# Performance work log

Measured on AMD Instinct MI355X. Metric: run time of the kernel, lower is better.

The kernel has to match this reference:

```python
import jax, jax.numpy as jnp
import numpy as np

B, S, E = 8, 8192, 1024  # batch, seq_len, embed_dim (= n_wires)


def _rx(psi, th):
    # psi: (E, 2) complex64, th: scalar/(1,)/(E,)
    c = jnp.cos(0.5 * th)
    s = jnp.sin(0.5 * th)
    a, b = psi[..., 0], psi[..., 1]
    return jnp.stack([c * a - 1j * s * b, -1j * s * a + c * b], axis=-1)


def _ry(psi, th):
    c = jnp.cos(0.5 * th)
    s = jnp.sin(0.5 * th)
    a, b = psi[..., 0], psi[..., 1]
    return jnp.stack([c * a - s * b, s * a + c * b], axis=-1)


def _rz(psi, th):
    p = jnp.exp(-0.5j * th.astype(jnp.complex64))
    a, b = psi[..., 0], psi[..., 1]
    return jnp.stack([p * a, jnp.conj(p) * b], axis=-1)


def setup_inputs() -> dict:
    key = jax.random.key(0)
    ks = jax.random.split(key, 9)
    return {
        "x": jax.random.normal(ks[0], (B, S, E), dtype=jnp.float32),
        "bs_theta": jax.random.normal(ks[1], (1,), dtype=jnp.float32) * 0.5,
        "bs_phi": jax.random.normal(ks[2], (1,), dtype=jnp.float32) * 0.5,
        "phases": jax.random.normal(ks[3], (E,), dtype=jnp.float32),
        "squeeze_r": jax.random.normal(ks[4], (E,), dtype=jnp.float32),
        "displacement_r": jax.random.normal(ks[5], (E,), dtype=jnp.float32),
        "kerr": jax.random.normal(ks[6], (E,), dtype=jnp.float32),
        "W_combine": jax.random.normal(ks[7], (E, E), dtype=jnp.float32) / np.sqrt(E),
        "b_combine": jax.random.normal(ks[8], (E,), dtype=jnp.float32) * 0.01,
    }


def reference(x, bs_theta, bs_phi, phases, squeeze_r, displacement_r, kerr,
              W_combine, b_combine):
    e = x.shape[-1]
    # One qubit per embedding wire, all starting at |0>; gates are single-wire,
    # so the 2^E product state factorizes exactly into (E, 2) amplitudes.
    psi = jnp.zeros((e, 2), dtype=jnp.complex64).at[:, 0].set(1.0)
    psi = _rx(psi, bs_theta)          # rx(bs_theta) on every wire
    psi = _ry(psi, bs_phi)            # ry(bs_phi)
    psi = _rz(psi, phases)            # rz(phases[i])
    psi = _ry(psi, squeeze_r)         # ry(squeeze_r[i])
    psi = _rx(psi, displacement_r)    # rx(displacement_r[i])
    psi = _rz(psi, kerr)              # rz(kerr[i])
    # MeasureAll(PauliZ): <Z_i> = |a_i|^2 - |b_i|^2, shape (E,)
    z = (jnp.abs(psi[:, 0]) ** 2 - jnp.abs(psi[:, 1]) ** 2).astype(x.dtype)
    # Device is reset per token/batch; measurement is input-independent,
    # so the (single) head output is z broadcast over (B, S).
    head_out = jnp.broadcast_to(z, x.shape)  # (B, S, E)
    return jnp.einsum('bse,fe->bsf', head_out, W_combine) + b_combine
```

## Files before the change

### kernel.cpp

```cpp
#include <hip/hip_runtime.h>
#include <hip/hip_bf16.h>


#define E 1024

__global__ void zvec_kernel(const float* __restrict__ bs_theta,
                            const float* __restrict__ bs_phi,
                            const float* __restrict__ phases,
                            const float* __restrict__ squeeze_r,
                            const float* __restrict__ displacement_r,
                            float* __restrict__ z) {
    int e = blockIdx.x * blockDim.x + threadIdx.x;
    if (e >= E) return;

    float h1 = 0.5f * bs_theta[0];
    float c1 = cosf(h1), s1 = sinf(h1);
    float h2 = 0.5f * bs_phi[0];
    float c2 = cosf(h2), s2 = sinf(h2);
    float ar = c2 * c1, ai = s2 * s1;
    float br = s2 * c1, bi = -c2 * s1;

    float hp = 0.5f * phases[e];
    float pr = cosf(hp), pi = -sinf(hp);
    float nar = ar * pr - ai * pi, nai = ar * pi + ai * pr;
    float nbr = br * pr + bi * pi, nbi = bi * pr - br * pi;
    ar = nar; ai = nai; br = nbr; bi = nbi;

    float hs = 0.5f * squeeze_r[e];
    float cs = cosf(hs), ss = sinf(hs);
    nar = cs * ar - ss * br; nai = cs * ai - ss * bi;
    nbr = ss * ar + cs * br; nbi = ss * ai + cs * bi;
    ar = nar; ai = nai; br = nbr; bi = nbi;

    float hd = 0.5f * displacement_r[e];
    float cd = cosf(hd), sd = sinf(hd);
    nar = cd * ar + sd * bi; nai = cd * ai - sd * br;
    nbr = sd * ai + cd * br; nbi = cd * bi - sd * ar;

    z[e] = (nar * nar + nai * nai) - (nbr * nbr + nbi * nbi);
}

__global__ void matvec_kernel(const float* __restrict__ W,
                              const float* __restrict__ z,
                              const float* __restrict__ bias,
                              float* __restrict__ y) {
    int f = blockIdx.x;
    const float* row = W + (size_t)f * E;
    float p = 0.f;
    for (int e = threadIdx.x; e < E; e += 256) p += row[e] * z[e];
    #pragma unroll
    for (int o = 32; o > 0; o >>= 1) p += __shfl_down(p, o, 64);
    __shared__ float sm[4];
    int lane = threadIdx.x & 63, wv = threadIdx.x >> 6;
    if (lane == 0) sm[wv] = p;
    __syncthreads();
    if (threadIdx.x == 0) y[f] = sm[0] + sm[1] + sm[2] + sm[3] + bias[f];
}

__global__ void __launch_bounds__(256)
bcast_kernel(const float* __restrict__ y, float4* __restrict__ out, long n4) {
    __shared__ float4 sy[E / 4];
    for (int i = threadIdx.x; i < E / 4; i += 256)
        sy[i] = ((const float4*)y)[i];
    __syncthreads();
    long stride = (long)gridDim.x * 256;
    for (long i = (long)blockIdx.x * 256 + threadIdx.x; i < n4; i += stride)
        out[i] = sy[i & (E / 4 - 1)];
}

extern "C" void kernel_launch(void* const* d_in, const int* in_sizes, int n_in,
                              void* d_out, int out_size, void* d_ws, size_t ws_size,
                              hipStream_t stream) {
    const float* bs_theta       = (const float*)d_in[1];
    const float* bs_phi         = (const float*)d_in[2];
    const float* phases         = (const float*)d_in[3];
    const float* squeeze_r      = (const float*)d_in[4];
    const float* displacement_r = (const float*)d_in[5];
    const float* W_combine      = (const float*)d_in[7];
    const float* b_combine      = (const float*)d_in[8];

    float* z = (float*)d_ws;
    float* y = z + E;

    zvec_kernel<<<1, E, 0, stream>>>(bs_theta, bs_phi, phases, squeeze_r,
                                     displacement_r, z);
    matvec_kernel<<<E, 256, 0, stream>>>(W_combine, z, b_combine, y);

    long n4 = (long)out_size / 4;
    int grid = 16384;
    bcast_kernel<<<grid, 256, 0, stream>>>(y, (float4*)d_out, n4);
}
```

Before: 400.4 us.

## Fuse z-vector computation into matvec and simplify broadcast store kernel

Merges the z-vector kernel into the matvec kernel: each of the 1024 blocks recomputes all 1024 z values into shared memory and then does a float4 dot product with its W row, removing one launch. The broadcast kernel drops the grid-stride loop and shared-memory staging; each thread holds one float4 of y in a register and writes 8 rows. This trades redundant trig work per block for fewer launches and simpler store addressing. The output is 256 MB of writes, so store bandwidth still dominates.

```diff
diff --git a/kernel.cpp b/kernel.cpp
--- a/kernel.cpp
+++ b/kernel.cpp
@@ -4,50 +4,56 @@
 
 #define E 1024
 
-__global__ void zvec_kernel(const float* __restrict__ bs_theta,
-                            const float* __restrict__ bs_phi,
-                            const float* __restrict__ phases,
-                            const float* __restrict__ squeeze_r,
-                            const float* __restrict__ displacement_r,
-                            float* __restrict__ z) {
-    int e = blockIdx.x * blockDim.x + threadIdx.x;
-    if (e >= E) return;
+__global__ void __launch_bounds__(256)
+y_kernel(const float* __restrict__ bs_theta,
+         const float* __restrict__ bs_phi,
+         const float* __restrict__ phases,
+         const float* __restrict__ squeeze_r,
+         const float* __restrict__ displacement_r,
+         const float* __restrict__ W,
+         const float* __restrict__ bias,
+         float* __restrict__ y) {
+    __shared__ float zs[E];
 
     float h1 = 0.5f * bs_theta[0];
     float c1 = cosf(h1), s1 = sinf(h1);
     float h2 = 0.5f * bs_phi[0];
     float c2 = cosf(h2), s2 = sinf(h2);
-    float ar = c2 * c1, ai = s2 * s1;
-    float br = s2 * c1, bi = -c2 * s1;
+    float ar0 = c2 * c1, ai0 = s2 * s1;
+    float br0 = s2 * c1, bi0 = -c2 * s1;
 
-    float hp = 0.5f * phases[e];
-    float pr = cosf(hp), pi = -sinf(hp);
-    float nar = ar * pr - ai * pi, nai = ar * pi + ai * pr;
-    float nbr = br * pr + bi * pi, nbi = bi * pr - br * pi;
-    ar = nar; ai = nai; br = nbr; bi = nbi;
+    #pragma unroll
+    for (int k = 0; k < E / 256; ++k) {
+        int e = threadIdx.x + k * 256;
+        float ar = ar0, ai = ai0, br = br0, bi = bi0;
 
-    float hs = 0.5f * squeeze_r[e];
-    float cs = cosf(hs), ss = sinf(hs);
-    nar = cs * ar - ss * br; nai = cs * ai - ss * bi;
-    nbr = ss * ar + cs * br; nbi = ss * ai + cs * bi;
-    ar = nar; ai = nai; br = nbr; bi = nbi;
+        float hp = 0.5f * phases[e];
+        float pr = cosf(hp), pi = -sinf(hp);
+        float nar = ar * pr - ai * pi, nai = ar * pi + ai * pr;
+        float nbr = br * pr + bi * pi, nbi = bi * pr - br * pi;
+        ar = nar; ai = nai; br = nbr; bi = nbi;
 
-    float hd = 0.5f * displacement_r[e];
-    float cd = cosf(hd), sd = sinf(hd);
-    nar = cd * ar + sd * bi; nai = cd * ai - sd * br;
-    nbr = sd * ai + cd * br; nbi = cd * bi - sd * ar;
+        float hs = 0.5f * squeeze_r[e];
+        float cs = cosf(hs), ss = sinf(hs);
+        nar = cs * ar - ss * br; nai = cs * ai - ss * bi;
+        nbr = ss * ar + cs * br; nbi = ss * ai + cs * bi;
+        ar = nar; ai = nai; br = nbr; bi = nbi;
 
-    z[e] = (nar * nar + nai * nai) - (nbr * nbr + nbi * nbi);
-}
+        float hd = 0.5f * displacement_r[e];
+        float cd = cosf(hd), sd = sinf(hd);
+        nar = cd * ar + sd * bi; nai = cd * ai - sd * br;
+        nbr = sd * ai + cd * br; nbi = cd * bi - sd * ar;
 
-__global__ void matvec_kernel(const float* __restrict__ W,
-                              const float* __restrict__ z,
-                              const float* __restrict__ bias,
-                              float* __restrict__ y) {
+        zs[e] = (nar * nar + nai * nai) - (nbr * nbr + nbi * nbi);
+    }
+    __syncthreads();
+
     int f = blockIdx.x;
-    const float* row = W + (size_t)f * E;
-    float p = 0.f;
-    for (int e = threadIdx.x; e < E; e += 256) p += row[e] * z[e];
+    const float4* row4 = (const float4*)(W + (size_t)f * E);
+    float4 w = row4[threadIdx.x];
+    float4 zv = ((const float4*)zs)[threadIdx.x];
+    float p = w.x * zv.x + w.y * zv.y + w.z * zv.z + w.w * zv.w;
+
     #pragma unroll
     for (int o = 32; o > 0; o >>= 1) p += __shfl_down(p, o, 64);
     __shared__ float sm[4];
@@ -58,14 +64,13 @@
 }
 
 __global__ void __launch_bounds__(256)
-bcast_kernel(const float* __restrict__ y, float4* __restrict__ out, long n4) {
-    __shared__ float4 sy[E / 4];
-    for (int i = threadIdx.x; i < E / 4; i += 256)
-        sy[i] = ((const float4*)y)[i];
-    __syncthreads();
-    long stride = (long)gridDim.x * 256;
-    for (long i = (long)blockIdx.x * 256 + threadIdx.x; i < n4; i += stride)
-        out[i] = sy[i & (E / 4 - 1)];
+bcast_kernel(const float4* __restrict__ y4, float4* __restrict__ out,
+             int rows_per_block) {
+    float4 v = y4[threadIdx.x];
+    long base = (long)blockIdx.x * rows_per_block * (E / 4) + threadIdx.x;
+    #pragma unroll 4
+    for (int r = 0; r < rows_per_block; ++r)
+        out[base + (long)r * (E / 4)] = v;
 }
 
 extern "C" void kernel_launch(void* const* d_in, const int* in_sizes, int n_in,
@@ -79,14 +84,14 @@
     const float* W_combine      = (const float*)d_in[7];
     const float* b_combine      = (const float*)d_in[8];
 
-    float* z = (float*)d_ws;
-    float* y = z + E;
+    float* y = (float*)d_ws;
 
-    zvec_kernel<<<1, E, 0, stream>>>(bs_theta, bs_phi, phases, squeeze_r,
-                                     displacement_r, z);
-    matvec_kernel<<<E, 256, 0, stream>>>(W_combine, z, b_combine, y);
+    y_kernel<<<E, 256, 0, stream>>>(bs_theta, bs_phi, phases, squeeze_r,
+                                    displacement_r, W_combine, b_combine, y);
 
-    long n4 = (long)out_size / 4;
-    int grid = 16384;
-    bcast_kernel<<<grid, 256, 0, stream>>>(y, (float4*)d_out, n4);
+    int rows = out_size / E;
+    int rows_per_block = 8;
+    int grid = rows / rows_per_block;
+    bcast_kernel<<<grid, 256, 0, stream>>>((const float4*)y, (float4*)d_out,
+                                           rows_per_block);
 }
```

New measurement: 399.6 us. About the same (-0.2%).
